# Optimization experiments

Hardware: AMD Instinct MI355X
Metric: run time of the kernel (lower is better)

The kernel has to match this reference:

```python
import jax, jax.numpy as jnp
import numpy as np

EMBED_DIM = 1024
PROJ_DIM = 128
B = 32
S = 1024


def setup_inputs() -> dict:
    key = jax.random.key(0)
    k1, k2, k3 = jax.random.split(key, 3)
    context = jax.random.normal(k1, (S, B, EMBED_DIM), jnp.float32)  # [seq, batch, embed]
    prior = jax.random.uniform(k2, (B, S), dtype=jnp.float32)
    padding_mask = jnp.zeros((B, S), jnp.int32)
    # xavier_uniform for proj_weight [2*proj_dim, embed_dim]
    bound = float(np.sqrt(6.0 / (2 * PROJ_DIM + EMBED_DIM)))
    proj_weight = jax.random.uniform(k3, (2 * PROJ_DIM, EMBED_DIM), jnp.float32, -bound, bound)
    proj_bias = jnp.zeros((2 * PROJ_DIM,), jnp.float32)
    return {"context": context, "prior": prior, "padding_mask": padding_mask,
            "proj_weight": proj_weight, "proj_bias": proj_bias}


def reference(context, prior, padding_mask, proj_weight, proj_bias):
    ctx = jnp.transpose(context, (1, 0, 2))  # [B, S, E]
    b, s, e = ctx.shape
    qk = ctx @ proj_weight.T + proj_bias  # [B, S, 2*proj_dim]
    query, key = jnp.split(qk, 2, axis=2)
    # neighbor scores (note: original divides by embed_dim, not proj_dim)
    fwd = jnp.sum(query[:, :-1] * key[:, 1:], axis=-1) / e    # [B, S-1]
    bwd = jnp.sum(query[:, 1:] * key[:, :-1], axis=-1) / e    # [B, S-1]
    ninf = jnp.full((b, 1), -jnp.inf, ctx.dtype)
    col0 = jnp.concatenate([fwd, ninf], axis=1)   # score[:, :, 0]
    col1 = jnp.concatenate([ninf, bwd], axis=1)   # score[:, :, 1]
    rolled_mask = jnp.roll(padding_mask, -1, axis=1)
    col0 = jnp.where(rolled_mask == 1, -jnp.inf, col0)
    prob = jax.nn.softmax(jnp.stack([col0, col1], axis=-1), axis=-1)  # [B, S, 2]
    # torch .roll with no dims flattens first -- replicate exactly
    shift_prob = jnp.roll(prob[:, :, 1].reshape(-1), -1).reshape(b, s)
    p = jnp.sqrt(prob[:, :, 0] * shift_prob + 1e-6)
    neighbor_attn = prior + (1 - prior) * p  # [B, S]
    log_prob = jnp.log(neighbor_attn)
    log_prob = jnp.where(rolled_mask == 1, 0.0, log_prob)
    # The two triangular bmms compute C[i,j] = sum_{k=i}^{j-1} log_prob[k] for j>i.
    # Equivalent O(S^2) form via exclusive prefix sum of log_prob[:, :-1].
    csp = jnp.concatenate([jnp.zeros((b, 1), ctx.dtype),
                           jnp.cumsum(log_prob[:, :-1], axis=1)], axis=1)  # [B, S]
    diff = csp[:, None, :] - csp[:, :, None]  # diff[b,i,j] = csp[j] - csp[i]
    upper = jnp.triu(diff, k=1)
    constituent_attn = jnp.exp(upper + jnp.swapaxes(upper, 1, 2))
    constituent_attn = jnp.where(jnp.eye(s, dtype=bool), 0.0, constituent_attn)
    return constituent_attn, neighbor_attn
```

## Files before the change

### kernel.cpp

```cpp
#include <hip/hip_runtime.h>
#include <hip/hip_bf16.h>
#include <math.h>

#define EMB 1024
#define BATCH 32
#define SEQ 1024
#define J2 256
#define BM 64
#define BN 256
#define BK 64

typedef __attribute__((ext_vector_type(8))) short short8;
typedef __attribute__((ext_vector_type(4))) float f32x4;
typedef const __attribute__((address_space(1))) void gvoid;
typedef __attribute__((address_space(3))) void lvoid;

union Pack8 { short8 s; __hip_bfloat16 h[8]; };

__global__ __launch_bounds__(256) void convw(const float* __restrict__ W,
                                             __hip_bfloat16* __restrict__ Wb) {
    int i = blockIdx.x * 256 + threadIdx.x;
    float4 v = ((const float4*)W)[i];
    __hip_bfloat16 h[4];
    h[0] = __float2bfloat16(v.x); h[1] = __float2bfloat16(v.y);
    h[2] = __float2bfloat16(v.z); h[3] = __float2bfloat16(v.w);
    *(short4*)&Wb[i * 4] = *(short4*)h;
}

__global__ __launch_bounds__(256) void gemm_mfma(const float* __restrict__ ctx,
                                                 const __hip_bfloat16* __restrict__ Wb,
                                                 const float* __restrict__ bias,
                                                 float* __restrict__ qk) {
    __shared__ __align__(16) __hip_bfloat16 As[BM * BK];
    __shared__ __align__(16) __hip_bfloat16 Bs[BN * BK];
    const int t = threadIdx.x;
    const int lane = t & 63, w = t >> 6;
    const int m0 = blockIdx.x * BM;
    const int wn = w * 64;
    const int lm = lane & 15, lq = lane >> 4;

    f32x4 acc[4][4] = {};

    float bv[4];
    #pragma unroll
    for (int ni = 0; ni < 4; ni++) bv[ni] = bias[wn + ni * 16 + lm];

    const float4* ctx4 = (const float4*)ctx;

    for (int k0 = 0; k0 < EMB; k0 += BK) {
        #pragma unroll
        for (int c = 0; c < 8; c++) {
            int li = c * 256 + t;
            int row = li >> 3, k8 = li & 7;
            const __hip_bfloat16* g = Wb + (size_t)row * EMB + k0 + k8 * 8;
            __hip_bfloat16* l = &Bs[(c * 256 + w * 64) * 8];
            __builtin_amdgcn_global_load_lds((gvoid*)g, (lvoid*)l, 16, 0, 0);
        }
        const int k4 = k0 >> 2;
        #pragma unroll
        for (int c = 0; c < 2; c++) {
            int li = c * 256 + t;
            int row = li >> 3, k8 = li & 7;
            float4 v0 = ctx4[(size_t)(m0 + row) * 256 + k4 + k8 * 2];
            float4 v1 = ctx4[(size_t)(m0 + row) * 256 + k4 + k8 * 2 + 1];
            Pack8 p;
            p.h[0] = __float2bfloat16(v0.x); p.h[1] = __float2bfloat16(v0.y);
            p.h[2] = __float2bfloat16(v0.z); p.h[3] = __float2bfloat16(v0.w);
            p.h[4] = __float2bfloat16(v1.x); p.h[5] = __float2bfloat16(v1.y);
            p.h[6] = __float2bfloat16(v1.z); p.h[7] = __float2bfloat16(v1.w);
            *(short8*)&As[row * BK + k8 * 8] = p.s;
        }
        __syncthreads();
        #pragma unroll
        for (int kk = 0; kk < BK; kk += 32) {
            short8 af[4], bfr[4];
            #pragma unroll
            for (int i = 0; i < 4; i++) {
                af[i]  = *(const short8*)&As[(i * 16 + lm) * BK + kk + lq * 8];
                bfr[i] = *(const short8*)&Bs[(wn + i * 16 + lm) * BK + kk + lq * 8];
            }
            #pragma unroll
            for (int mi = 0; mi < 4; mi++)
                #pragma unroll
                for (int ni = 0; ni < 4; ni++)
                    acc[mi][ni] = __builtin_amdgcn_mfma_f32_16x16x32_bf16(
                        af[mi], bfr[ni], acc[mi][ni], 0, 0, 0);
        }
        __syncthreads();
    }

    #pragma unroll
    for (int mi = 0; mi < 4; mi++) {
        #pragma unroll
        for (int r = 0; r < 4; r++) {
            int m = m0 + mi * 16 + lq * 4 + r;
            int s = m >> 5, b = m & 31;
            float* orow = qk + (size_t)((b << 10) + s) * J2;
            #pragma unroll
            for (int ni = 0; ni < 4; ni++) {
                int n = wn + ni * 16 + lm;
                orow[n] = acc[mi][ni][r] + bv[ni];
            }
        }
    }
}

__global__ __launch_bounds__(256) void scores(const float* __restrict__ qk,
                                              float* __restrict__ fwd,
                                              float* __restrict__ bwd) {
    int wave = threadIdx.x >> 6, lane = threadIdx.x & 63;
    int idx = blockIdx.x * 4 + wave;
    int s = idx & (SEQ - 1);
    if (s == SEQ - 1) return;
    const float* row0 = qk + (size_t)idx * J2;
    const float* row1 = row0 + J2;
    float f = row0[lane] * row1[128 + lane] + row0[64 + lane] * row1[192 + lane];
    float w = row1[lane] * row0[128 + lane] + row1[64 + lane] * row0[192 + lane];
    #pragma unroll
    for (int off = 32; off; off >>= 1) {
        f += __shfl_xor(f, off);
        w += __shfl_xor(w, off);
    }
    if (lane == 0) {
        fwd[idx] = f * (1.f / 1024.f);
        bwd[idx] = w * (1.f / 1024.f);
    }
}

__global__ __launch_bounds__(1024) void neighbor(const float* __restrict__ fwd,
                                                 const float* __restrict__ bwd,
                                                 const float* __restrict__ prior,
                                                 const int* __restrict__ mask,
                                                 float* __restrict__ out_n,
                                                 float* __restrict__ csp) {
    int b = blockIdx.x, s = threadIdx.x;
    __shared__ float p1s[SEQ];
    __shared__ float buf[2][SEQ];
    int base = b << 10;
    int rolled = mask[base + ((s + 1) & (SEQ - 1))];
    float c0 = (s < SEQ - 1) ? fwd[base + s] : -INFINITY;
    if (rolled) c0 = -INFINITY;
    float c1 = (s > 0) ? bwd[base + s - 1] : -INFINITY;
    float m = fmaxf(c0, c1);
    float e0 = expf(c0 - m), e1 = expf(c1 - m);
    float inv = 1.f / (e0 + e1);
    float p0 = e0 * inv, p1 = e1 * inv;
    p1s[s] = p1;
    __syncthreads();
    float shift = (s < SEQ - 1) ? p1s[s + 1] : 0.f;
    float p = sqrtf(p0 * shift + 1e-6f);
    float pr = prior[base + s];
    float na = pr + (1.f - pr) * p;
    out_n[base + s] = na;
    float lp = logf(na);
    if (rolled) lp = 0.f;
    buf[0][s] = lp;
    __syncthreads();
    int cur = 0;
    for (int off = 1; off < SEQ; off <<= 1) {
        float v = buf[cur][s];
        if (s >= off) v += buf[cur][s - off];
        buf[cur ^ 1][s] = v;
        __syncthreads();
        cur ^= 1;
    }
    csp[base + s] = (s == 0) ? 0.f : buf[cur][s - 1];
}

__global__ __launch_bounds__(256) void outk(const float* __restrict__ csp,
                                            float* __restrict__ out) {
    int bi = blockIdx.x;
    int b = bi >> 10, i = bi & (SEQ - 1);
    const float* crow = csp + (b << 10);
    float ci = crow[i];
    int t = threadIdx.x;
    float4 cj = ((const float4*)crow)[t];
    int j0 = t << 2;
    float4 r;
    {
        int j = j0 + 0;
        r.x = (j == i) ? 0.f : expf((j > i) ? (cj.x - ci) : (ci - cj.x));
        j = j0 + 1;
        r.y = (j == i) ? 0.f : expf((j > i) ? (cj.y - ci) : (ci - cj.y));
        j = j0 + 2;
        r.z = (j == i) ? 0.f : expf((j > i) ? (cj.z - ci) : (ci - cj.z));
        j = j0 + 3;
        r.w = (j == i) ? 0.f : expf((j > i) ? (cj.w - ci) : (ci - cj.w));
    }
    ((float4*)(out + (size_t)bi * SEQ))[t] = r;
}

extern "C" void kernel_launch(void* const* d_in, const int* in_sizes, int n_in,
                              void* d_out, int out_size, void* d_ws, size_t ws_size,
                              hipStream_t stream) {
    (void)in_sizes; (void)n_in; (void)out_size; (void)ws_size;
    const float* ctx   = (const float*)d_in[0];
    const float* prior = (const float*)d_in[1];
    const int*   mask  = (const int*)d_in[2];
    const float* W     = (const float*)d_in[3];
    const float* bias  = (const float*)d_in[4];
    float* out = (float*)d_out;
    float* ws  = (float*)d_ws;

    float* qk  = ws;
    float* fwd = ws + 8388608;
    float* bwd = fwd + 32768;
    float* csp = bwd + 32768;
    __hip_bfloat16* Wb = (__hip_bfloat16*)(csp + 32768);
    float* out_n = out + (size_t)BATCH * SEQ * SEQ;

    convw    <<<256, 256, 0, stream>>>(W, Wb);
    gemm_mfma<<<(BATCH * SEQ) / BM, 256, 0, stream>>>(ctx, Wb, bias, qk);
    scores   <<<(BATCH * SEQ) / 4, 256, 0, stream>>>(qk, fwd, bwd);
    neighbor <<<BATCH, 1024, 0, stream>>>(fwd, bwd, prior, mask, out_n, csp);
    outk     <<<BATCH * SEQ, 256, 0, stream>>>(csp, out);
}
```

Baseline: 272.0 us.

## Store qk as bf16, use perm-based bf16 packing, and warp-shuffle scan

The GEMM now writes its qk intermediate in bf16 instead of fp32, which halves the write and the subsequent read traffic in the scores kernel. The fp32-to-bf16 conversion of the context tile is replaced by a byte-permute with round-half-up bias instead of round-to-nearest-even. The neighbor kernel's 10-step shared-memory Hillis-Steele scan is replaced by a wave-level shuffle scan plus a per-wave offset pass, which cuts the number of block barriers. These changes lower precision in qk and in rounding, which can affect accuracy of the neighbour scores.

```diff
diff --git a/kernel.cpp b/kernel.cpp
--- a/kernel.cpp
+++ b/kernel.cpp
@@ -9,13 +9,19 @@
 #define BM 64
 #define BN 256
 #define BK 64
+#define PSEL 0x07060302u
 
 typedef __attribute__((ext_vector_type(8))) short short8;
 typedef __attribute__((ext_vector_type(4))) float f32x4;
 typedef const __attribute__((address_space(1))) void gvoid;
 typedef __attribute__((address_space(3))) void lvoid;
 
-union Pack8 { short8 s; __hip_bfloat16 h[8]; };
+__device__ __forceinline__ unsigned bcast(float f) {
+    union { float f; unsigned u; } c; c.f = f; return c.u;
+}
+__device__ __forceinline__ unsigned pack_bf16(float f0, float f1) {
+    return __builtin_amdgcn_perm(bcast(f1) + 0x8000u, bcast(f0) + 0x8000u, PSEL);
+}
 
 __global__ __launch_bounds__(256) void convw(const float* __restrict__ W,
                                              __hip_bfloat16* __restrict__ Wb) {
@@ -30,7 +36,7 @@
 __global__ __launch_bounds__(256) void gemm_mfma(const float* __restrict__ ctx,
                                                  const __hip_bfloat16* __restrict__ Wb,
                                                  const float* __restrict__ bias,
-                                                 float* __restrict__ qk) {
+                                                 __hip_bfloat16* __restrict__ qkb) {
     __shared__ __align__(16) __hip_bfloat16 As[BM * BK];
     __shared__ __align__(16) __hip_bfloat16 Bs[BN * BK];
     const int t = threadIdx.x;
@@ -63,12 +69,12 @@
             int row = li >> 3, k8 = li & 7;
             float4 v0 = ctx4[(size_t)(m0 + row) * 256 + k4 + k8 * 2];
             float4 v1 = ctx4[(size_t)(m0 + row) * 256 + k4 + k8 * 2 + 1];
-            Pack8 p;
-            p.h[0] = __float2bfloat16(v0.x); p.h[1] = __float2bfloat16(v0.y);
-            p.h[2] = __float2bfloat16(v0.z); p.h[3] = __float2bfloat16(v0.w);
-            p.h[4] = __float2bfloat16(v1.x); p.h[5] = __float2bfloat16(v1.y);
-            p.h[6] = __float2bfloat16(v1.z); p.h[7] = __float2bfloat16(v1.w);
-            *(short8*)&As[row * BK + k8 * 8] = p.s;
+            uint4 p;
+            p.x = pack_bf16(v0.x, v0.y);
+            p.y = pack_bf16(v0.z, v0.w);
+            p.z = pack_bf16(v1.x, v1.y);
+            p.w = pack_bf16(v1.z, v1.w);
+            *(uint4*)&As[row * BK + k8 * 8] = p;
         }
         __syncthreads();
         #pragma unroll
@@ -95,27 +101,33 @@
         for (int r = 0; r < 4; r++) {
             int m = m0 + mi * 16 + lq * 4 + r;
             int s = m >> 5, b = m & 31;
-            float* orow = qk + (size_t)((b << 10) + s) * J2;
+            __hip_bfloat16* orow = qkb + (size_t)((b << 10) + s) * J2;
             #pragma unroll
             for (int ni = 0; ni < 4; ni++) {
                 int n = wn + ni * 16 + lm;
-                orow[n] = acc[mi][ni][r] + bv[ni];
+                orow[n] = __float2bfloat16(acc[mi][ni][r] + bv[ni]);
             }
         }
     }
 }
 
-__global__ __launch_bounds__(256) void scores(const float* __restrict__ qk,
+__global__ __launch_bounds__(256) void scores(const __hip_bfloat16* __restrict__ qkb,
                                               float* __restrict__ fwd,
                                               float* __restrict__ bwd) {
     int wave = threadIdx.x >> 6, lane = threadIdx.x & 63;
     int idx = blockIdx.x * 4 + wave;
     int s = idx & (SEQ - 1);
     if (s == SEQ - 1) return;
-    const float* row0 = qk + (size_t)idx * J2;
-    const float* row1 = row0 + J2;
-    float f = row0[lane] * row1[128 + lane] + row0[64 + lane] * row1[192 + lane];
-    float w = row1[lane] * row0[128 + lane] + row1[64 + lane] * row0[192 + lane];
+    const unsigned* r0 = (const unsigned*)(qkb + (size_t)idx * J2);
+    const unsigned* r1 = r0 + 128;
+    unsigned q0 = r0[lane], k0 = r0[64 + lane];
+    unsigned q1 = r1[lane], k1 = r1[64 + lane];
+    float2 q0f = __bfloat1622float2(*(const __hip_bfloat162*)&q0);
+    float2 k0f = __bfloat1622float2(*(const __hip_bfloat162*)&k0);
+    float2 q1f = __bfloat1622float2(*(const __hip_bfloat162*)&q1);
+    float2 k1f = __bfloat1622float2(*(const __hip_bfloat162*)&k1);
+    float f = q0f.x * k1f.x + q0f.y * k1f.y;
+    float w = q1f.x * k0f.x + q1f.y * k0f.y;
     #pragma unroll
     for (int off = 32; off; off >>= 1) {
         f += __shfl_xor(f, off);
@@ -134,8 +146,10 @@
                                                  float* __restrict__ out_n,
                                                  float* __restrict__ csp) {
     int b = blockIdx.x, s = threadIdx.x;
+    int lane = s & 63, w = s >> 6;
     __shared__ float p1s[SEQ];
-    __shared__ float buf[2][SEQ];
+    __shared__ float incl[SEQ];
+    __shared__ float wsum[16];
     int base = b << 10;
     int rolled = mask[base + ((s + 1) & (SEQ - 1))];
     float c0 = (s < SEQ - 1) ? fwd[base + s] : -INFINITY;
@@ -154,17 +168,28 @@
     out_n[base + s] = na;
     float lp = logf(na);
     if (rolled) lp = 0.f;
-    buf[0][s] = lp;
-    __syncthreads();
-    int cur = 0;
-    for (int off = 1; off < SEQ; off <<= 1) {
-        float v = buf[cur][s];
-        if (s >= off) v += buf[cur][s - off];
-        buf[cur ^ 1][s] = v;
-        __syncthreads();
-        cur ^= 1;
-    }
-    csp[base + s] = (s == 0) ? 0.f : buf[cur][s - 1];
+    float x = lp;
+    #pragma unroll
+    for (int off = 1; off < 64; off <<= 1) {
+        float v = __shfl_up(x, off);
+        if (lane >= off) x += v;
+    }
+    if (lane == 63) wsum[w] = x;
+    __syncthreads();
+    if (w == 0) {
+        float v = (lane < 16) ? wsum[lane] : 0.f;
+        #pragma unroll
+        for (int off = 1; off < 16; off <<= 1) {
+            float t2 = __shfl_up(v, off);
+            if (lane >= off) v += t2;
+        }
+        if (lane < 16) wsum[lane] = v;
+    }
+    __syncthreads();
+    float woff = (w > 0) ? wsum[w - 1] : 0.f;
+    incl[s] = x + woff;
+    __syncthreads();
+    csp[base + s] = (s == 0) ? 0.f : incl[s - 1];
 }
 
 __global__ __launch_bounds__(256) void outk(const float* __restrict__ csp,
@@ -202,16 +227,16 @@
     float* out = (float*)d_out;
     float* ws  = (float*)d_ws;
 
-    float* qk  = ws;
-    float* fwd = ws + 8388608;
+    __hip_bfloat16* qkb = (__hip_bfloat16*)ws;
+    float* fwd = ws + 4194304;
     float* bwd = fwd + 32768;
     float* csp = bwd + 32768;
     __hip_bfloat16* Wb = (__hip_bfloat16*)(csp + 32768);
     float* out_n = out + (size_t)BATCH * SEQ * SEQ;
 
     convw    <<<256, 256, 0, stream>>>(W, Wb);
-    gemm_mfma<<<(BATCH * SEQ) / BM, 256, 0, stream>>>(ctx, Wb, bias, qk);
-    scores   <<<(BATCH * SEQ) / 4, 256, 0, stream>>>(qk, fwd, bwd);
+    gemm_mfma<<<(BATCH * SEQ) / BM, 256, 0, stream>>>(ctx, Wb, bias, qkb);
+    scores   <<<(BATCH * SEQ) / 4, 256, 0, stream>>>(qkb, fwd, bwd);
     neighbor <<<BATCH, 1024, 0, stream>>>(fwd, bwd, prior, mask, out_n, csp);
     outk     <<<BATCH * SEQ, 256, 0, stream>>>(csp, out);
 }
```

After: 268.1 us. About the same (-1.4%).
